# Kernel optimization log

Measured on AMD Instinct MI355X. Metric: run time of the kernel, lower is better.

## Reference

```python
import jax, jax.numpy as jnp
import numpy as np

C, H, D = 64, 2, 32
NQ, NA, NE, F_IN = 8192, 32768, 500000, 128
E_E2Q, E_E2E, E_E2A, E_Q2A = 131072, 800000, 262144, 32768
N_POS, N_NEG = 8192, 24576
# node types: 0=question, 1=answer, 2=entity
# edge types (src_type, dst_type): e2q=(2,0), e2e=(2,2), e2a=(2,1), q2a=(0,1)
REL_ST = [(2, 0), (2, 2), (2, 1), (0, 1)]


def _edges(k, n_src, n_dst, e):
    k1, k2 = jax.random.split(k)
    return jnp.stack([jax.random.randint(k1, (e,), 0, n_src),
                      jax.random.randint(k2, (e,), 0, n_dst)]).astype(jnp.int32)


def setup_inputs():
    key = jax.random.key(0)
    ks = jax.random.split(key, 16)
    inp = {
        'x_question': jax.random.normal(ks[0], (NQ, F_IN), jnp.float32),
        'x_answer': jax.random.normal(ks[1], (NA, F_IN), jnp.float32),
        'x_entity': jax.random.normal(ks[2], (NE, F_IN), jnp.float32),
        'e_e2q': _edges(ks[3], NE, NQ, E_E2Q),
        'e_e2e': _edges(ks[4], NE, NE, E_E2E),
        'e_e2a': _edges(ks[5], NE, NA, E_E2A),
        'e_q2a': _edges(ks[6], NQ, NA, E_Q2A),
        'pos_idx': _edges(ks[7], NQ, NA, N_POS),
        'neg_idx': _edges(ks[8], NQ, NA, N_NEG),
        # learned parameters (stacked over the 3 node types / 4 edge types)
        'W_in': jax.random.normal(ks[9], (3, F_IN, C), jnp.float32) / np.sqrt(F_IN).astype(np.float32),
        'b_in': jnp.zeros((3, C), jnp.float32),
        'bn_gamma': jnp.ones((3, C), jnp.float32),
        'bn_beta': jnp.zeros((3, C), jnp.float32),
        'W_kqv': jax.random.normal(ks[10], (3, C, 3 * C), jnp.float32) / np.sqrt(C).astype(np.float32),
        'b_kqv': jnp.zeros((3, 3 * C), jnp.float32),
        'A_k': jax.random.normal(ks[11], (4, H, D, D), jnp.float32) / np.sqrt(D).astype(np.float32),
        'A_v': jax.random.normal(ks[12], (4, H, D, D), jnp.float32) / np.sqrt(D).astype(np.float32),
        'p_rel': jnp.ones((4, H), jnp.float32),
        'W_out': jax.random.normal(ks[13], (3, C, C), jnp.float32) / np.sqrt(C).astype(np.float32),
        'b_out': jnp.zeros((3, C), jnp.float32),
        'skip': jnp.ones((3,), jnp.float32),
    }
    return inp


def _segment_attn(scores, vals, dst, n):
    # scores [E,H], vals [E,H,D]: softmax over incoming edges per dst node, weighted scatter-add
    m = jax.ops.segment_max(scores, dst, num_segments=n)          # [N,H]
    e = jnp.exp(scores - m[dst])                                   # [E,H]
    s = jax.ops.segment_sum(e, dst, num_segments=n)                # [N,H]
    w = e / s[dst]
    return jax.ops.segment_sum(vals * w[..., None], dst, num_segments=n)  # [N,H,D]


def _forward(x_question, x_answer, x_entity, W_in, b_in, bn_gamma, bn_beta,
             W_kqv, b_kqv, A_k, A_v, p_rel, W_out, b_out, skip, edges):
    xs = [x_question, x_answer, x_entity]
    h = []
    for t in range(3):
        y = jax.nn.relu(xs[t] @ W_in[t] + b_in[t])
        mu = y.mean(0)
        var = y.var(0)  # biased, as in torch BN training mode
        y = bn_gamma[t] * (y - mu) * jax.lax.rsqrt(var + 1e-5) + bn_beta[t]
        h.append(y)
    kqv = [h[t] @ W_kqv[t] + b_kqv[t] for t in range(3)]
    k = [kv[:, :C].reshape(-1, H, D) for kv in kqv]
    q = [kv[:, C:2 * C].reshape(-1, H, D) for kv in kqv]
    v = [kv[:, 2 * C:].reshape(-1, H, D) for kv in kqv]
    by_dst = {0: [], 1: [], 2: []}
    inv_sqrt_d = jnp.float32(1.0 / np.sqrt(D))
    for r, ((st, dt), ei) in enumerate(zip(REL_ST, edges)):
        src, dst = ei[0], ei[1]
        k_r = jnp.einsum('ehd,hdf->ehf', k[st][src], A_k[r])   # per-relation key transform
        v_r = jnp.einsum('ehd,hdf->ehf', v[st][src], A_v[r])   # per-relation value transform
        sc = (q[dt][dst] * k_r).sum(-1) * p_rel[r] * inv_sqrt_d  # [E,H]
        by_dst[dt].append((sc, v_r, dst))
    out = []
    for t in range(3):
        sc = jnp.concatenate([a for a, _, _ in by_dst[t]], axis=0)
        vr = jnp.concatenate([b for _, b, _ in by_dst[t]], axis=0)
        dst = jnp.concatenate([c for _, _, c in by_dst[t]], axis=0)
        n = h[t].shape[0]
        agg = _segment_attn(sc, vr, dst, n).reshape(n, C)
        a = jax.nn.gelu(agg, approximate=False) @ W_out[t] + b_out[t]
        g = jax.nn.sigmoid(skip[t])
        out.append(g * a + (1.0 - g) * h[t])
    return out  # [z_question, z_answer, z_entity]


def reference(x_question, x_answer, x_entity, e_e2q, e_e2e, e_e2a, e_q2a,
              pos_idx, neg_idx, W_in, b_in, bn_gamma, bn_beta, W_kqv, b_kqv,
              A_k, A_v, p_rel, W_out, b_out, skip):
    zq, za, ze = _forward(x_question, x_answer, x_entity, W_in, b_in, bn_gamma,
                          bn_beta, W_kqv, b_kqv, A_k, A_v, p_rel, W_out, b_out,
                          skip, [e_e2q, e_e2e, e_e2a, e_q2a])
    pos_pred = (zq[pos_idx[0]] * za[pos_idx[1]]).sum(-1)
    neg_pred = (zq[neg_idx[0]] * za[neg_idx[1]]).sum(-1)
    return pos_pred, neg_pred, zq, za, ze
```

## Files before the change

### kernel.cpp

```cpp
#include <hip/hip_runtime.h>
#include <hip/hip_bf16.h>
#include <hip/hip_fp16.h>
#include <math.h>

#define NQ 8192
#define NA 32768
#define NE 500000
#define F_IN 128
#define E_E2Q 131072
#define E_E2E 800000
#define E_E2A 262144
#define E_Q2A 32768
#define N_POS 8192
#define N_NEG 24576

#define NT_TOTAL (NQ + NA + NE)
#define E_TOTAL (E_E2Q + E_E2E + E_E2A + E_Q2A)
#define NBLK_SCAN ((NT_TOTAL + 1023) / 1024)
#define CDIV(a, b) (((a) + (b) - 1) / (b))

#define BASE_Q 0
#define BASE_A NQ
#define BASE_E (NQ + NA)

#define GIN_Q 128
#define GIN_A 512
#define GIN_E 768
#define SMEM_INPROJ (32768 + 17408 + 512)

#define GB_Q 2048
#define GB_E 4096
#define GB_A 8192

typedef _Float16 half8_t __attribute__((ext_vector_type(8)));
typedef _Float16 half4_t __attribute__((ext_vector_type(4)));
typedef _Float16 half2_t __attribute__((ext_vector_type(2)));
typedef float f32x4_t __attribute__((ext_vector_type(4)));

__device__ inline void load_lds16(const void* g, void* l) {
  __builtin_amdgcn_global_load_lds((const __attribute__((address_space(1))) void*)g,
                                   (__attribute__((address_space(3))) void*)l, 16, 0, 0);
}

__device__ inline float fast_gelu(float v) {
  float u = 1.5957691216057308f * fmaf(0.044715f * v * v, v, v);
  return v / (1.f + __expf(-u));
}


__global__ __launch_bounds__(256) void prep_misc(
    float* __restrict__ row_start_f,
    const float* __restrict__ W_in, _Float16* __restrict__ WinT,
    const float* __restrict__ W_out, _Float16* __restrict__ WoutT)
{
  int bid = blockIdx.x;
  if (bid < 128) {
    size_t i = (size_t)bid * 256 + threadIdx.x;
    size_t stride = (size_t)128 * 256;
    for (; i < NT_TOTAL; i += stride) row_start_f[i] = 0.f;
  } else if (bid < 320) {
    int b = bid - 128;
    int t = b >> 6, n = b & 63, k = threadIdx.x;
    if (k < 136) {
      float v = (k < 128) ? W_in[(size_t)t * 128 * 64 + (size_t)k * 64 + n] : 0.f;
      WinT[((size_t)t * 64 + n) * 136 + k] = (_Float16)v;
    }
  } else {
    int b = bid - 320;
    int t = b >> 6, n = b & 63, k = threadIdx.x;
    if (k < 72) {
      float v = (k < 64) ? W_out[(size_t)t * 64 * 64 + (size_t)k * 64 + n] : 0.f;
      WoutT[((size_t)t * 64 + n) * 72 + k] = (_Float16)v;
    }
  }
}


__global__ __launch_bounds__(256) void gemm_inproj(
    const float* __restrict__ Af, const _Float16* __restrict__ WT,
    const float* __restrict__ bias, int M, int ntiles,
    _Float16* __restrict__ oh, float* __restrict__ bstats)
{
  extern __shared__ char smem[];
  float* As32 = (float*)smem;
  _Float16* Bs = (_Float16*)(smem + 32768);
  float* s1 = (float*)(smem + 32768 + 17408);
  float* s2 = s1 + 64;

  int tid = threadIdx.x;
  int w = tid >> 6, l = tid & 63;
  int lr = l & 15, lg = l >> 4;

  for (int idx = tid; idx < 64 * 136 / 8; idx += 256)
    *(half8_t*)&Bs[idx * 8] = *(const half8_t*)&WT[(size_t)idx * 8];
  if (tid < 64) { s1[tid] = 0.f; s2[tid] = 0.f; }

  float ps1[4] = {}, ps2[4] = {};
  float bval[4];
#pragma unroll
  for (int ct = 0; ct < 4; ++ct) bval[ct] = bias[ct * 16 + lr];

  for (int tile = blockIdx.x; tile < ntiles; tile += gridDim.x) {
    const char* srcbase = (const char*)Af + (size_t)tile * 64 * 512;
    int rowlim = M - tile * 64;
#pragma unroll
    for (int r = 0; r < 8; ++r) {
      int unit = r * 4 + w;
      char* ldst = (char*)As32 + unit * 1024;
      int p = unit * 1024 + l * 16;
      int row = p >> 9;
      const char* src = (row < rowlim) ? srcbase + (size_t)row * 512 + (p & 511)
                                       : srcbase;
      load_lds16(src, ldst);
    }
    __syncthreads();

    f32x4_t acc[4] = {};
#pragma unroll
    for (int ks = 0; ks < 4; ++ks) {
      const float4* pa = (const float4*)((const char*)As32 +
                          (w * 16 + lr) * 512 + ks * 128 + lg * 32);
      float4 x0 = pa[0], x1 = pa[1];
      half8_t a0 = {(_Float16)x0.x, (_Float16)x0.y, (_Float16)x0.z, (_Float16)x0.w,
                    (_Float16)x1.x, (_Float16)x1.y, (_Float16)x1.z, (_Float16)x1.w};
#pragma unroll
      for (int ct = 0; ct < 4; ++ct) {
        half8_t b = *(const half8_t*)&Bs[(ct * 16 + lr) * 136 + ks * 32 + lg * 8];
        acc[ct] = __builtin_amdgcn_mfma_f32_16x16x32_f16(a0, b, acc[ct], 0, 0, 0);
      }
    }

    int rbase = tile * 64 + w * 16 + lg * 4;
#pragma unroll
    for (int ct = 0; ct < 4; ++ct) {
      int col = ct * 16 + lr;
#pragma unroll
      for (int j = 0; j < 4; ++j) {
        int row = rbase + j;
        if (row >= M) continue;
        float val = fmaxf(acc[ct][j] + bval[ct], 0.f);
        oh[(size_t)row * 64 + col] = (_Float16)val;
        ps1[ct] += val;
        ps2[ct] += val * val;
      }
    }
    __syncthreads();
  }

#pragma unroll
  for (int ct = 0; ct < 4; ++ct) {
    atomicAdd(&s1[ct * 16 + lr], ps1[ct]);
    atomicAdd(&s2[ct * 16 + lr], ps2[ct]);
  }
  __syncthreads();
  if (tid < 64) {
    bstats[(size_t)blockIdx.x * 128 + tid] = s1[tid];
    bstats[(size_t)blockIdx.x * 128 + 64 + tid] = s2[tid];
  }
}


template <int BNT, int KTOT, int MODE>
__global__ __launch_bounds__(256) void gemm_direct(
    const float* __restrict__ Af, const _Float16* __restrict__ Ah,
    const _Float16* __restrict__ WT, const float* __restrict__ bias, int M,
    _Float16* __restrict__ oh, int LDO,
    float* __restrict__ Cf,
    float* __restrict__ bstats,
    const _Float16* __restrict__ resh, const float* __restrict__ rsc,
    const float* __restrict__ rsh, const float* __restrict__ skip_ptr, int skip_idx)
{
  constexpr int KP = KTOT + 8;
  __shared__ _Float16 Bs[BNT * KP];
  int tid = threadIdx.x;
  int w = tid >> 6, l = tid & 63;
  int lr = l & 15, lg = l >> 4;
  int row0 = blockIdx.x * 128;

  for (int idx = tid; idx < BNT * KP / 8; idx += 256)
    *(half8_t*)&Bs[idx * 8] = *(const half8_t*)&WT[(size_t)idx * 8];

  constexpr int NKS = KTOT / 32;
  half8_t afrag[2][NKS];
#pragma unroll
  for (int rt = 0; rt < 2; ++rt) {
    int gr = row0 + w * 32 + rt * 16 + lr;
    bool ok = gr < M;
#pragma unroll
    for (int ks = 0; ks < NKS; ++ks) {
      half8_t h8 = {};
      if (ok) h8 = *(const half8_t*)&Ah[(size_t)gr * KTOT + ks * 32 + lg * 8];
      afrag[rt][ks] = h8;
    }
  }
  __syncthreads();

  constexpr int NCT = BNT / 16;
  f32x4_t acc[2][NCT] = {};
#pragma unroll
  for (int ks = 0; ks < NKS; ++ks) {
#pragma unroll
    for (int ct = 0; ct < NCT; ++ct) {
      half8_t b = *(const half8_t*)&Bs[(ct * 16 + lr) * KP + ks * 32 + lg * 8];
      acc[0][ct] = __builtin_amdgcn_mfma_f32_16x16x32_f16(afrag[0][ks], b, acc[0][ct], 0, 0, 0);
      acc[1][ct] = __builtin_amdgcn_mfma_f32_16x16x32_f16(afrag[1][ks], b, acc[1][ct], 0, 0, 0);
    }
  }

  float g = 1.f / (1.f + __expf(-skip_ptr[skip_idx]));
  float gb = 1.f - g;
#pragma unroll
  for (int rt = 0; rt < 2; ++rt) {
    int rbase = row0 + w * 32 + rt * 16 + lg * 4;
#pragma unroll
    for (int ct = 0; ct < NCT; ++ct) {
      int col = ct * 16 + lr;
      float bval = bias[col];
#pragma unroll
      for (int j = 0; j < 4; ++j) {
        int row = rbase + j;
        if (row >= M) continue;
        float val = acc[rt][ct][j] + bval;
        float rv = (float)resh[(size_t)row * 64 + col];
        Cf[(size_t)row * 64 + col] = g * val + gb * (rsc[col] * rv + rsh[col]);
      }
    }
  }
}


template <int BM, int BNT, int KTOT>
__global__ __launch_bounds__(BM * 2) void gemm_mfma(
    const _Float16* __restrict__ Ah,
    const _Float16* __restrict__ WT, const float* __restrict__ bias, int M,
    _Float16* __restrict__ oh, int LDO)
{
  constexpr int KP = KTOT + 8;
  constexpr int NTHR = BM * 2;
  constexpr int TP = BNT + 8;
  constexpr int SZ_AB = (BM * KP + BNT * KP) * 2;
  constexpr int SZ_T = 128 * TP * 2;
  constexpr int SZ = SZ_AB > SZ_T ? SZ_AB : SZ_T;
  __shared__ __align__(16) char smem[SZ];
  _Float16* As = (_Float16*)smem;
  _Float16* Bs = As + BM * KP;
  _Float16* Ts = (_Float16*)smem;
  int tid = threadIdx.x;
  int row0 = blockIdx.x * BM;
  int colbase = blockIdx.y * BNT;

  {
    constexpr int CH = KTOT / 8;
    for (int idx = tid; idx < BM * CH; idx += NTHR) {
      int row = idx / CH, c = idx % CH;
      int gr = row0 + row;
      half8_t a8 = {};
      if (gr < M) a8 = *(const half8_t*)&Ah[(size_t)gr * KTOT + c * 8];
      *(half8_t*)&As[row * KP + c * 8] = a8;
    }
  }
  {
    const _Float16* wsrc = WT + (size_t)colbase * KP;
    for (int idx = tid; idx < BNT * KP / 8; idx += NTHR)
      *(half8_t*)&Bs[idx * 8] = *(const half8_t*)&wsrc[(size_t)idx * 8];
  }
  __syncthreads();

  int w = tid >> 6, l = tid & 63;
  int lr = l & 15, lg = l >> 4;
  constexpr int NCT = BNT / 16;
  constexpr int NKS = KTOT / 32;
  f32x4_t acc[2][NCT] = {};
#pragma unroll
  for (int ks = 0; ks < NKS; ++ks) {
    half8_t a0 = *(const half8_t*)&As[(w * 32 + lr) * KP + ks * 32 + lg * 8];
    half8_t a1 = *(const half8_t*)&As[(w * 32 + 16 + lr) * KP + ks * 32 + lg * 8];
#pragma unroll
    for (int ct = 0; ct < NCT; ++ct) {
      half8_t b = *(const half8_t*)&Bs[(ct * 16 + lr) * KP + ks * 32 + lg * 8];
      acc[0][ct] = __builtin_amdgcn_mfma_f32_16x16x32_f16(a0, b, acc[0][ct], 0, 0, 0);
      acc[1][ct] = __builtin_amdgcn_mfma_f32_16x16x32_f16(a1, b, acc[1][ct], 0, 0, 0);
    }
  }

  float bval[NCT];
#pragma unroll
  for (int ct = 0; ct < NCT; ++ct) bval[ct] = bias[colbase + ct * 16 + lr];

#pragma unroll
  for (int rt = 0; rt < 2; ++rt) {
    __syncthreads();
    int r2base = w * 16 + lg * 4;
#pragma unroll
    for (int ct = 0; ct < NCT; ++ct) {
      int colL = ct * 16 + lr;
#pragma unroll
      for (int j = 0; j < 4; ++j)
        Ts[(r2base + j) * TP + colL] = (_Float16)(acc[rt][ct][j] + bval[ct]);
    }
    __syncthreads();
    constexpr int C8 = BNT / 8;
    for (int idx = tid; idx < 128 * C8; idx += NTHR) {
      int r2 = idx / C8, c8 = (idx % C8) * 8;
      int gr = row0 + (r2 >> 4) * 32 + rt * 16 + (r2 & 15);
      if (gr < M)
        *(half8_t*)&oh[(size_t)gr * LDO + colbase + c8] = *(const half8_t*)&Ts[r2 * TP + c8];
    }
  }
}


__global__ __launch_bounds__(256) void stats_reduce(const float* __restrict__ bstats,
                                                    float* __restrict__ stats) {
  __shared__ float sh[256];
  int t = blockIdx.x >> 7;
  int c = blockIdx.x & 127;
  int nb = (t == 0) ? GIN_Q : (t == 1) ? GIN_A : GIN_E;
  int base = (t == 0) ? 0 : (t == 1) ? GIN_Q : (GIN_Q + GIN_A);
  float s = 0.f;
  for (int i = threadIdx.x; i < nb; i += 256)
    s += bstats[(size_t)(base + i) * 128 + c];
  sh[threadIdx.x] = s;
  __syncthreads();
  for (int off2 = 128; off2 > 0; off2 >>= 1) {
    if (threadIdx.x < off2) sh[threadIdx.x] += sh[threadIdx.x + off2];
    __syncthreads();
  }
  if (threadIdx.x == 0) stats[t * 128 + c] = sh[0];
}

__global__ void bn_finalize(const float* __restrict__ stats,
                            const float* __restrict__ gamma, const float* __restrict__ beta,
                            float* __restrict__ scale, float* __restrict__ shift) {
  int t = threadIdx.x;
  if (t >= 192) return;
  int ty = t >> 6, c = t & 63;
  float invN = (ty == 0) ? (1.f / NQ) : (ty == 1) ? (1.f / NA) : (1.f / NE);
  float mu = stats[ty * 128 + c] * invN;
  float var = stats[ty * 128 + 64 + c] * invN - mu * mu;
  float rs = rsqrtf(var + 1e-5f);
  float gm = gamma[ty * 64 + c];
  scale[t] = gm * rs;
  shift[t] = beta[ty * 64 + c] - gm * mu * rs;
}

__global__ void kqv_bias2(const float* __restrict__ b_kqv, const float* __restrict__ W_kqv,
                          const float* __restrict__ shift, float* __restrict__ bias2) {
  int t = blockIdx.x, n = threadIdx.x;
  float s = b_kqv[t * 192 + n];
  for (int k = 0; k < 64; ++k)
    s += shift[t * 64 + k] * W_kqv[(size_t)t * 64 * 192 + k * 192 + n];
  bias2[t * 192 + n] = s;
}


__global__ void wprep_kqv(const float* __restrict__ W_kqv, const float* __restrict__ bias2,
                          const float* __restrict__ A_k, const float* __restrict__ A_v,
                          const float* __restrict__ scale,
                          _Float16* __restrict__ WqT, _Float16* __restrict__ WeT,
                          _Float16* __restrict__ WaT, float* __restrict__ bias_big) {
  int j = blockIdx.x;
  int c = threadIdx.x;
  int t, jj, bofs;
  _Float16* W;
  if (j < 192)      { t = 0; jj = j;       W = WqT; bofs = 0; }
  else if (j < 512) { t = 2; jj = j - 192; W = WeT; bofs = 192; }
  else              { t = 1; jj = j - 512; W = WaT; bofs = 512; }
  const float* Wt = W_kqv + (size_t)t * 64 * 192;
  const float* b2 = bias2 + t * 192;
  int mode = 0, rel = 0, sub = 0;
  if (t == 1) { mode = 1; rel = (jj < 64) ? 2 : 3; sub = jj & 63; }
  else if (jj >= 64 && jj < 128) { mode = 1; rel = (t == 0) ? 0 : 1; sub = jj - 64; }
  else if (jj >= 128) {
    mode = 2; sub = (jj - 128) & 63;
    rel = (t == 0) ? 3 : ((jj - 128) >> 6);
  }
  int h = sub >> 5, x = sub & 31;
  float wv, bv;
  if (mode == 0) {
    wv = Wt[(size_t)c * 192 + jj];
    bv = b2[jj];
  } else if (mode == 1) {
    const float* Ar = A_k + ((size_t)rel * 2048 + h * 1024 + x * 32);
    float s = 0.f, sb = 0.f;
    for (int f = 0; f < 32; ++f) {
      float a = Ar[f];
      s = fmaf(a, Wt[(size_t)c * 192 + 64 + h * 32 + f], s);
      sb = fmaf(a, b2[64 + h * 32 + f], sb);
    }
    wv = s; bv = sb;
  } else {
    const float* Ar = A_v + ((size_t)rel * 2048 + h * 1024 + x);
    float s = 0.f, sb = 0.f;
    for (int d = 0; d < 32; ++d) {
      float a = Ar[d * 32];
      s = fmaf(a, Wt[(size_t)c * 192 + 128 + h * 32 + d], s);
      sb = fmaf(a, b2[128 + h * 32 + d], sb);
    }
    wv = s; bv = sb;
  }
  wv *= scale[t * 64 + c];
  W[(size_t)jj * 72 + c] = (_Float16)wv;
  if (c < 8) W[(size_t)jj * 72 + 64 + c] = (_Float16)0.f;
  if (c == 0) bias_big[bofs + jj] = bv;
}


__global__ __launch_bounds__(256) void hist_all(
    const int* __restrict__ d0, const int* __restrict__ d1,
    const int* __restrict__ d2, const int* __restrict__ d3,
    unsigned* __restrict__ cnt)
{
  int i = blockIdx.x * blockDim.x + threadIdx.x;
  int stride = gridDim.x * blockDim.x;
  for (; i < E_TOTAL; i += stride) {
    if (i < E_E2Q) atomicAdd(&cnt[BASE_Q + d0[i]], 1u);
    else if (i < E_E2Q + E_E2E) atomicAdd(&cnt[BASE_E + d1[i - E_E2Q]], 1u);
    else if (i < E_E2Q + E_E2E + E_E2A) atomicAdd(&cnt[BASE_A + d2[i - E_E2Q - E_E2E]], 1u);
    else atomicAdd(&cnt[BASE_A + d3[i - E_E2Q - E_E2E - E_E2A]], 1u);
  }
}

__global__ __launch_bounds__(256) void scan1(unsigned* __restrict__ arr, int n,
                                             unsigned* __restrict__ bsums) {
  __shared__ unsigned sh[256];
  int t = threadIdx.x;
  int base = blockIdx.x * 1024 + t * 4;
  unsigned v[4];
  unsigned s = 0;
#pragma unroll
  for (int j = 0; j < 4; ++j) {
    v[j] = (base + j < n) ? arr[base + j] : 0u;
    s += v[j];
  }
  sh[t] = s;
  __syncthreads();
  for (int off = 1; off < 256; off <<= 1) {
    unsigned x = (t >= off) ? sh[t - off] : 0u;
    __syncthreads();
    sh[t] += x;
    __syncthreads();
  }
  unsigned run = sh[t] - s;
#pragma unroll
  for (int j = 0; j < 4; ++j) {
    if (base + j < n) arr[base + j] = run;
    run += v[j];
  }
  if (t == 255) bsums[blockIdx.x] = sh[255];
}

__global__ __launch_bounds__(256) void scan2(unsigned* __restrict__ bsums, int nb) {
  __shared__ unsigned sh[256];
  __shared__ unsigned carry;
  int t = threadIdx.x;
  if (t == 0) carry = 0;
  __syncthreads();
  for (int chunk = 0; chunk < nb; chunk += 256) {
    int i = chunk + t;
    unsigned v = (i < nb) ? bsums[i] : 0u;
    sh[t] = v;
    __syncthreads();
    for (int off = 1; off < 256; off <<= 1) {
      unsigned x = (t >= off) ? sh[t - off] : 0u;
      __syncthreads();
      sh[t] += x;
      __syncthreads();
    }
    unsigned inc = sh[t];
    unsigned c = carry;
    __syncthreads();
    if (i < nb) bsums[i] = c + inc - v;
    if (t == 255) carry = c + sh[255];
    __syncthreads();
  }
}

__global__ __launch_bounds__(256) void scan3(unsigned* __restrict__ arr,
                                             const unsigned* __restrict__ bsums,
                                             unsigned* __restrict__ cursor, int n) {
  int t = threadIdx.x;
  int base = blockIdx.x * 1024 + t * 4;
  unsigned add = bsums[blockIdx.x];
#pragma unroll
  for (int j = 0; j < 4; ++j) {
    int idx = base + j;
    if (idx < n) {
      unsigned r = arr[idx] + add;
      arr[idx] = r;
      cursor[idx] = r;
    }
  }
}

__global__ __launch_bounds__(256) void scatter_all(
    const int* __restrict__ s0, const int* __restrict__ d0,
    const int* __restrict__ s1, const int* __restrict__ d1,
    const int* __restrict__ s2, const int* __restrict__ d2,
    const int* __restrict__ s3, const int* __restrict__ d3,
    unsigned* __restrict__ cursor, unsigned* __restrict__ eidx)
{
  int i = blockIdx.x * blockDim.x + threadIdx.x;
  int stride = gridDim.x * blockDim.x;
  for (; i < E_TOTAL; i += stride) {
    unsigned pos, pay;
    if (i < E_E2Q) {
      pos = atomicAdd(&cursor[BASE_Q + d0[i]], 1u);
      pay = (unsigned)(s0[i] * 320);
    } else if (i < E_E2Q + E_E2E) {
      int k = i - E_E2Q;
      pos = atomicAdd(&cursor[BASE_E + d1[k]], 1u);
      pay = (unsigned)(s1[k] * 320);
    } else if (i < E_E2Q + E_E2E + E_E2A) {
      int k = i - E_E2Q - E_E2E;
      pos = atomicAdd(&cursor[BASE_A + d2[k]], 1u);
      pay = (unsigned)(s2[k] * 320);
    } else {
      int k = i - E_E2Q - E_E2E - E_E2A;
      pos = atomicAdd(&cursor[BASE_A + d3[k]], 1u);
      pay = (unsigned)(s3[k] * 192) | 0x80000000u;
    }
    eidx[pos] = pay;
  }
}


template <int NREL>
__device__ __forceinline__ void gather_body(
    int bidLocal, int nblocks, int N, int nodebase,
    const unsigned* __restrict__ row_start, const unsigned* __restrict__ row_end,
    const unsigned* __restrict__ eidx,
    const _Float16* __restrict__ baseA, int vofA,
    const _Float16* __restrict__ baseB, int vofB,
    const _Float16* __restrict__ qtA, int ldqA,
    const _Float16* __restrict__ qtB, int ldqB,
    const float* __restrict__ prelA, const float* __restrict__ prelB,
    _Float16* __restrict__ agg)
{
  int lane = threadIdx.x & 63;
  int h = lane >> 5, f = lane & 31;
  int idx2 = h * 32 + 2 * (f & 15);
  const float isd = 0.17677669529663687f;
  float pr0 = prelA[h] * isd;
  float pr1 = (NREL == 2) ? prelB[h] * isd : 0.f;

  int wid = (int)(((size_t)bidLocal * 256 + threadIdx.x) >> 6);
  int nw = nblocks * 4;

  int n0 = wid;
  unsigned b0s = 0, b0e = 0, e00 = 0, e01 = 0;
  half2_t q00p = {}, q01p = {};
  if (n0 < N) {
    b0s = row_start[nodebase + n0];
    b0e = row_end[nodebase + n0];
    q00p = *(const half2_t*)&qtA[(size_t)n0 * ldqA + idx2];
    if (NREL == 2) q01p = *(const half2_t*)&qtB[(size_t)n0 * ldqB + idx2];
    e00 = eidx[b0s];
    e01 = eidx[b0s + 1];
  }
  int n1 = n0 + nw;
  unsigned b1s = 0, b1e = 0;
  half2_t q10p = {}, q11p = {};
  if (n0 < N && n1 < N) {
    b1s = row_start[nodebase + n1];
    b1e = row_end[nodebase + n1];
    q10p = *(const half2_t*)&qtA[(size_t)n1 * ldqA + idx2];
    if (NREL == 2) q11p = *(const half2_t*)&qtB[(size_t)n1 * ldqB + idx2];
  }

  while (n0 < N) {
    unsigned e10 = 0, e11 = 0;
    if (n1 < N) {
      e10 = eidx[b1s];
      e11 = eidx[b1s + 1];
    }
    int n2 = n1 + nw;
    unsigned b2s = 0, b2e = 0;
    half2_t q20p = {}, q21p = {};
    if (n2 < N) {
      b2s = row_start[nodebase + n2];
      b2e = row_end[nodebase + n2];
      q20p = *(const half2_t*)&qtA[(size_t)n2 * ldqA + idx2];
      if (NREL == 2) q21p = *(const half2_t*)&qtB[(size_t)n2 * ldqB + idx2];
    }

    float vs = 0.f, ss = 0.f;
    unsigned i = b0s;

    auto do_pair = [&](unsigned p1, unsigned p2) {
      unsigned o1 = p1 & 0x7FFFFFFFu, o2 = p2 & 0x7FFFFFFFu;
      bool r1 = (NREL == 2) && (p1 >> 31);
      bool r2 = (NREL == 2) && (p2 >> 31);
      const _Float16* b1 = (r1 ? baseB : baseA) + o1;
      const _Float16* b2 = (r2 ? baseB : baseA) + o2;
      half2_t k21 = *(const half2_t*)&b1[idx2];
      float v1 = (float)b1[(r1 ? vofB : vofA) + lane];
      half2_t k22 = *(const half2_t*)&b2[idx2];
      float v2 = (float)b2[(r2 ? vofB : vofA) + lane];
      float sa = __builtin_amdgcn_fdot2(k21, r1 ? q01p : q00p, 0.f, false);
      float sb = __builtin_amdgcn_fdot2(k22, r2 ? q01p : q00p, 0.f, false);
#pragma unroll
      for (int off = 1; off <= 8; off <<= 1) {
        sa += __shfl_xor(sa, off, 32);
        sb += __shfl_xor(sb, off, 32);
      }
      float w1 = __expf(sa * (r1 ? pr1 : pr0));
      float w2 = __expf(sb * (r2 ? pr1 : pr0));
      ss += w1 + w2;
      vs = fmaf(w1, v1, vs);
      vs = fmaf(w2, v2, vs);
    };
    auto do_single = [&](unsigned p1) {
      unsigned o1 = p1 & 0x7FFFFFFFu;
      bool r1 = (NREL == 2) && (p1 >> 31);
      const _Float16* b1 = (r1 ? baseB : baseA) + o1;
      half2_t k21 = *(const half2_t*)&b1[idx2];
      float v1 = (float)b1[(r1 ? vofB : vofA) + lane];
      float sa = __builtin_amdgcn_fdot2(k21, r1 ? q01p : q00p, 0.f, false);
#pragma unroll
      for (int off = 1; off <= 8; off <<= 1) sa += __shfl_xor(sa, off, 32);
      float w1 = __expf(sa * (r1 ? pr1 : pr0));
      ss += w1;
      vs = fmaf(w1, v1, vs);
    };

    if (i + 2 <= b0e) { do_pair(e00, e01); i += 2; }
    else if (i < b0e) { do_single(e00); i = b0e; }
    for (; i + 2 <= b0e; i += 2) do_pair(eidx[i], eidx[i + 1]);
    if (i < b0e) do_single(eidx[i]);

    float val = (ss > 0.f) ? vs / ss : 0.f;
    val = fast_gelu(val);
    agg[((size_t)(nodebase + n0)) * 64 + lane] = (_Float16)val;

    n0 = n1; b0s = b1s; b0e = b1e; q00p = q10p; q01p = q11p; e00 = e10; e01 = e11;
    n1 = n2; b1s = b2s; b1e = b2e; q10p = q20p; q11p = q21p;
  }
}

__global__ __launch_bounds__(256) void gather_all(
    const unsigned* __restrict__ row_start, const unsigned* __restrict__ row_end,
    const unsigned* __restrict__ eidx,
    const _Float16* __restrict__ kqvQ, const _Float16* __restrict__ kqvE,
    const _Float16* __restrict__ kqvA,
    const float* __restrict__ p_rel, _Float16* __restrict__ agg)
{
  int bid = blockIdx.x;
  if (bid < GB_Q) {
    gather_body<1>(bid, GB_Q, NQ, BASE_Q, row_start, row_end, eidx,
                   kqvE, 128, kqvE, 128, kqvQ + 64, 192, kqvQ + 64, 192,
                   p_rel + 0, p_rel + 0, agg);
  } else if (bid < GB_Q + GB_E) {
    gather_body<1>(bid - GB_Q, GB_E, NE, BASE_E, row_start, row_end, eidx,
                   kqvE, 192, kqvE, 192, kqvE + 64, 320, kqvE + 64, 320,
                   p_rel + 2, p_rel + 2, agg);
  } else {
    gather_body<2>(bid - GB_Q - GB_E, GB_A, NA, BASE_A, row_start, row_end, eidx,
                   kqvE, 256, kqvQ, 128, kqvA, 128, kqvA + 64, 128,
                   p_rel + 4, p_rel + 6, agg);
  }
}


__global__ void pred_kernel(const int* __restrict__ qi, const int* __restrict__ ai, int Np,
                            const float* __restrict__ zq, const float* __restrict__ za,
                            float* __restrict__ outp) {
  int i = blockIdx.x * blockDim.x + threadIdx.x;
  if (i >= Np) return;
  const float4* a = (const float4*)(zq + (size_t)qi[i] * 64);
  const float4* b = (const float4*)(za + (size_t)ai[i] * 64);
  float ssum = 0.f;
#pragma unroll
  for (int j = 0; j < 16; ++j) {
    float4 x = a[j], y = b[j];
    ssum += x.x * y.x + x.y * y.y + x.z * y.z + x.w * y.w;
  }
  outp[i] = ssum;
}


extern "C" void kernel_launch(void* const* d_in, const int* in_sizes, int n_in,
                              void* d_out, int out_size, void* d_ws, size_t ws_size,
                              hipStream_t stream) {
  const float* xq = (const float*)d_in[0];
  const float* xa = (const float*)d_in[1];
  const float* xe = (const float*)d_in[2];
  const int* e_e2q = (const int*)d_in[3];
  const int* e_e2e = (const int*)d_in[4];
  const int* e_e2a = (const int*)d_in[5];
  const int* e_q2a = (const int*)d_in[6];
  const int* pos_idx = (const int*)d_in[7];
  const int* neg_idx = (const int*)d_in[8];
  const float* W_in = (const float*)d_in[9];
  const float* b_in = (const float*)d_in[10];
  const float* bn_gamma = (const float*)d_in[11];
  const float* bn_beta = (const float*)d_in[12];
  const float* W_kqv = (const float*)d_in[13];
  const float* b_kqv = (const float*)d_in[14];
  const float* A_k = (const float*)d_in[15];
  const float* A_v = (const float*)d_in[16];
  const float* p_rel = (const float*)d_in[17];
  const float* W_out = (const float*)d_in[18];
  const float* b_out = (const float*)d_in[19];
  const float* skip = (const float*)d_in[20];
  float* out = (float*)d_out;

  float* ws = (float*)d_ws;
  size_t off = 0;
  _Float16* y_h = (_Float16*)(ws + off);    off += (size_t)NT_TOTAL * 32;
  _Float16* kqvQ = (_Float16*)(ws + off);   off += (size_t)NQ * 96;
  _Float16* kqvE = (_Float16*)(ws + off);   off += (size_t)NE * 160;
  _Float16* kqvA = (_Float16*)(ws + off);   off += (size_t)NA * 64;
  _Float16* agg_h = (_Float16*)(ws + off);  off += (size_t)NT_TOTAL * 32;
  float* stats = ws + off;                  off += 384;
  float* scale = ws + off;                  off += 192;
  float* shift = ws + off;                  off += 192;
  float* bias2 = ws + off;                  off += 576;
  float* bias_big = ws + off;               off += 640;
  _Float16* WqT = (_Float16*)(ws + off);    off += 192 * 72 / 2;
  _Float16* WeT = (_Float16*)(ws + off);    off += 320 * 72 / 2;
  _Float16* WaT = (_Float16*)(ws + off);    off += 128 * 72 / 2;
  _Float16* WinT = (_Float16*)(ws + off);   off += 3 * 64 * 136 / 2;
  _Float16* WoutT = (_Float16*)(ws + off);  off += 3 * 64 * 72 / 2;
  float* bstats = ws + off;                 off += (size_t)(GIN_Q + GIN_A + GIN_E) * 128;
  unsigned* row_start = (unsigned*)(ws + off); off += NT_TOTAL;
  unsigned* cursor = (unsigned*)(ws + off);    off += NT_TOTAL;
  unsigned* bsums = (unsigned*)(ws + off);     off += 1024;
  unsigned* eidx = (unsigned*)(ws + off);      off += E_TOTAL + 8;

  const int Ns[3] = {NQ, NA, NE};
  const float* xs[3] = {xq, xa, xe};
  const int gin[3] = {GIN_Q, GIN_A, GIN_E};
  const int bb[3] = {0, GIN_Q, GIN_Q + GIN_A};
  _Float16* yhb[3] = {y_h, y_h + (size_t)NQ * 64, y_h + (size_t)(NQ + NA) * 64};
  _Float16* aggb[3] = {agg_h, agg_h + (size_t)NQ * 64, agg_h + (size_t)(NQ + NA) * 64};
  float* zq_out = out + (N_POS + N_NEG);
  float* zbase[3] = {zq_out, zq_out + (size_t)NQ * 64, zq_out + (size_t)(NQ + NA) * 64};

  prep_misc<<<dim3(512), dim3(256), 0, stream>>>((float*)row_start, W_in, WinT, W_out, WoutT);

  for (int t = 0; t < 3; ++t) {
    gemm_inproj<<<dim3(gin[t]), dim3(256), SMEM_INPROJ, stream>>>(
        xs[t], WinT + (size_t)t * 64 * 136, b_in + t * 64, Ns[t], CDIV(Ns[t], 64),
        yhb[t], bstats + (size_t)bb[t] * 128);
  }
  stats_reduce<<<dim3(384), dim3(256), 0, stream>>>(bstats, stats);
  bn_finalize<<<dim3(1), dim3(192), 0, stream>>>(stats, bn_gamma, bn_beta, scale, shift);
  kqv_bias2<<<dim3(3), dim3(192), 0, stream>>>(b_kqv, W_kqv, shift, bias2);
  wprep_kqv<<<dim3(640), dim3(64), 0, stream>>>(W_kqv, bias2, A_k, A_v, scale,
                                                WqT, WeT, WaT, bias_big);

  gemm_mfma<256, 192, 64><<<dim3(CDIV(NQ, 256)), dim3(512), 0, stream>>>(
      yhb[0], WqT, bias_big, NQ, kqvQ, 192);
  gemm_mfma<256, 160, 64><<<dim3(CDIV(NE, 256), 2), dim3(512), 0, stream>>>(
      yhb[2], WeT, bias_big + 192, NE, kqvE, 320);
  gemm_mfma<256, 128, 64><<<dim3(CDIV(NA, 256)), dim3(512), 0, stream>>>(
      yhb[1], WaT, bias_big + 512, NA, kqvA, 128);

  hist_all<<<dim3(2048), dim3(256), 0, stream>>>(
      e_e2q + E_E2Q, e_e2e + E_E2E, e_e2a + E_E2A, e_q2a + E_Q2A, row_start);
  scan1<<<dim3(NBLK_SCAN), dim3(256), 0, stream>>>(row_start, NT_TOTAL, bsums);
  scan2<<<dim3(1), dim3(256), 0, stream>>>(bsums, NBLK_SCAN);
  scan3<<<dim3(NBLK_SCAN), dim3(256), 0, stream>>>(row_start, bsums, cursor, NT_TOTAL);
  scatter_all<<<dim3(2048), dim3(256), 0, stream>>>(
      e_e2q, e_e2q + E_E2Q, e_e2e, e_e2e + E_E2E,
      e_e2a, e_e2a + E_E2A, e_q2a, e_q2a + E_Q2A, cursor, eidx);

  gather_all<<<dim3(GB_Q + GB_E + GB_A), dim3(256), 0, stream>>>(
      row_start, cursor, eidx, kqvQ, kqvE, kqvA, p_rel, agg_h);

  for (int t = 0; t < 3; ++t) {
    gemm_direct<64, 64, 3><<<dim3(CDIV(Ns[t], 128)), dim3(256), 0, stream>>>(
        nullptr, aggb[t], WoutT + (size_t)t * 64 * 72, b_out + t * 64, Ns[t],
        nullptr, 0, zbase[t], nullptr,
        yhb[t], scale + t * 64, shift + t * 64, skip, t);
  }

  pred_kernel<<<dim3(CDIV(N_POS, 256)), dim3(256), 0, stream>>>(
      pos_idx, pos_idx + N_POS, N_POS, zbase[0], zbase[1], out);
  pred_kernel<<<dim3(CDIV(N_NEG, 256)), dim3(256), 0, stream>>>(
      neg_idx, neg_idx + N_NEG, N_NEG, zbase[0], zbase[1], out + N_POS);
}
```

Before: 728.1 us.

## Merge per-type input/output GEMMs and double-buffer input projection loads

Replaces the three per-node-type input-projection launches with one kernel that dispatches on block index. It double-buffers 32-row input tiles in LDS, issuing async global-to-LDS loads for the next tile while computing the current one. The per-type output GEMM launches and the two prediction launches are likewise each merged into a single launch. The aim is to hide global load latency and cut launch overhead, at the cost of smaller per-iteration tiles and manual waitcnt/barrier synchronisation.

```diff
diff --git a/kernel.cpp b/kernel.cpp
--- a/kernel.cpp
+++ b/kernel.cpp
@@ -26,11 +26,14 @@
 #define GIN_Q 128
 #define GIN_A 512
 #define GIN_E 768
-#define SMEM_INPROJ (32768 + 17408 + 512)
 
 #define GB_Q 2048
 #define GB_E 4096
 #define GB_A 8192
+
+#define TOP_Q 64
+#define TOP_A 256
+#define TOP_E 3907
 
 typedef _Float16 half8_t __attribute__((ext_vector_type(8)));
 typedef _Float16 half4_t __attribute__((ext_vector_type(4)));
@@ -76,64 +79,94 @@
 }
 
 
-__global__ __launch_bounds__(256) void gemm_inproj(
-    const float* __restrict__ Af, const _Float16* __restrict__ WT,
-    const float* __restrict__ bias, int M, int ntiles,
-    _Float16* __restrict__ oh, float* __restrict__ bstats)
+__global__ __launch_bounds__(256) void gemm_inproj_all(
+    const float* __restrict__ xq, const float* __restrict__ xa,
+    const float* __restrict__ xe,
+    const _Float16* __restrict__ WinT, const float* __restrict__ b_in,
+    _Float16* __restrict__ y_h, float* __restrict__ bstats)
 {
-  extern __shared__ char smem[];
-  float* As32 = (float*)smem;
-  _Float16* Bs = (_Float16*)(smem + 32768);
-  float* s1 = (float*)(smem + 32768 + 17408);
-  float* s2 = s1 + 64;
-
-  int tid = threadIdx.x;
-  int w = tid >> 6, l = tid & 63;
+  __shared__ __align__(16) float bufA[32 * 128];
+  __shared__ __align__(16) float bufB[32 * 128];
+  __shared__ _Float16 Bs[64 * 136];
+  __shared__ float s1[64], s2[64];
+
+  int bid = blockIdx.x;
+  int t, lb, nb;
+  const float* Af;
+  _Float16* oh;
+  if (bid < GIN_Q)              { t = 0; lb = bid;                 nb = GIN_Q; Af = xq; oh = y_h; }
+  else if (bid < GIN_Q + GIN_A) { t = 1; lb = bid - GIN_Q;         nb = GIN_A; Af = xa; oh = y_h + (size_t)NQ * 64; }
+  else                          { t = 2; lb = bid - GIN_Q - GIN_A; nb = GIN_E; Af = xe; oh = y_h + (size_t)(NQ + NA) * 64; }
+  int M = (t == 0) ? NQ : (t == 1) ? NA : NE;
+  int nh = CDIV(M, 32);
+  const _Float16* WT = WinT + (size_t)t * 64 * 136;
+  const float* bias = b_in + t * 64;
+
+  int tid = threadIdx.x, w = tid >> 6, l = tid & 63;
   int lr = l & 15, lg = l >> 4;
+  int wrow = (w & 1) * 16;
+  int wcol = (w >> 1) * 32;
 
   for (int idx = tid; idx < 64 * 136 / 8; idx += 256)
     *(half8_t*)&Bs[idx * 8] = *(const half8_t*)&WT[(size_t)idx * 8];
   if (tid < 64) { s1[tid] = 0.f; s2[tid] = 0.f; }
 
-  float ps1[4] = {}, ps2[4] = {};
-  float bval[4];
-#pragma unroll
-  for (int ct = 0; ct < 4; ++ct) bval[ct] = bias[ct * 16 + lr];
-
-  for (int tile = blockIdx.x; tile < ntiles; tile += gridDim.x) {
-    const char* srcbase = (const char*)Af + (size_t)tile * 64 * 512;
-    int rowlim = M - tile * 64;
-#pragma unroll
-    for (int r = 0; r < 8; ++r) {
+  float bval[2];
+  bval[0] = bias[wcol + lr];
+  bval[1] = bias[wcol + 16 + lr];
+  float ps1[2] = {}, ps2[2] = {};
+
+  auto stage = [&](float* buf, int h) {
+    const char* srcbase = (const char*)Af + (size_t)h * 32 * 512;
+    int rowlim = M - h * 32;
+#pragma unroll
+    for (int r = 0; r < 4; ++r) {
       int unit = r * 4 + w;
-      char* ldst = (char*)As32 + unit * 1024;
+      char* ldst = (char*)buf + unit * 1024;
       int p = unit * 1024 + l * 16;
       int row = p >> 9;
       const char* src = (row < rowlim) ? srcbase + (size_t)row * 512 + (p & 511)
                                        : srcbase;
       load_lds16(src, ldst);
     }
-    __syncthreads();
-
-    f32x4_t acc[4] = {};
+  };
+
+  int h0 = lb;
+  if (h0 < nh) stage(bufA, h0);
+  __syncthreads();
+
+  float* cur = bufA;
+  float* nxt = bufB;
+  for (int h = h0; h < nh; h += nb) {
+    int h2 = h + nb;
+    bool more = h2 < nh;
+    if (more) {
+      stage(nxt, h2);
+      asm volatile("s_waitcnt vmcnt(4)" ::: "memory");
+    } else {
+      asm volatile("s_waitcnt vmcnt(0)" ::: "memory");
+    }
+    __builtin_amdgcn_sched_barrier(0);
+    __builtin_amdgcn_s_barrier();
+
+    f32x4_t acc[2] = {};
 #pragma unroll
     for (int ks = 0; ks < 4; ++ks) {
-      const float4* pa = (const float4*)((const char*)As32 +
-                          (w * 16 + lr) * 512 + ks * 128 + lg * 32);
+      const float4* pa = (const float4*)((const char*)cur +
+                          (wrow + lr) * 512 + ks * 128 + lg * 32);
       float4 x0 = pa[0], x1 = pa[1];
       half8_t a0 = {(_Float16)x0.x, (_Float16)x0.y, (_Float16)x0.z, (_Float16)x0.w,
                     (_Float16)x1.x, (_Float16)x1.y, (_Float16)x1.z, (_Float16)x1.w};
 #pragma unroll
-      for (int ct = 0; ct < 4; ++ct) {
-        half8_t b = *(const half8_t*)&Bs[(ct * 16 + lr) * 136 + ks * 32 + lg * 8];
+      for (int ct = 0; ct < 2; ++ct) {
+        half8_t b = *(const half8_t*)&Bs[(wcol + ct * 16 + lr) * 136 + ks * 32 + lg * 8];
         acc[ct] = __builtin_amdgcn_mfma_f32_16x16x32_f16(a0, b, acc[ct], 0, 0, 0);
       }
     }
-
-    int rbase = tile * 64 + w * 16 + lg * 4;
-#pragma unroll
-    for (int ct = 0; ct < 4; ++ct) {
-      int col = ct * 16 + lr;
+    int rbase = h * 32 + wrow + lg * 4;
+#pragma unroll
+    for (int ct = 0; ct < 2; ++ct) {
+      int col = wcol + ct * 16 + lr;
 #pragma unroll
       for (int j = 0; j < 4; ++j) {
         int row = rbase + j;
@@ -144,13 +177,15 @@
         ps2[ct] += val * val;
       }
     }
-    __syncthreads();
-  }
-
-#pragma unroll
-  for (int ct = 0; ct < 4; ++ct) {
-    atomicAdd(&s1[ct * 16 + lr], ps1[ct]);
-    atomicAdd(&s2[ct * 16 + lr], ps2[ct]);
+    __builtin_amdgcn_s_barrier();
+    float* tmp = cur; cur = nxt; nxt = tmp;
+  }
+
+#pragma unroll
+  for (int ct = 0; ct < 2; ++ct) {
+    int col = wcol + ct * 16 + lr;
+    atomicAdd(&s1[col], ps1[ct]);
+    atomicAdd(&s2[col], ps2[ct]);
   }
   __syncthreads();
   if (tid < 64) {
@@ -160,60 +195,66 @@
 }
 
 
-template <int BNT, int KTOT, int MODE>
-__global__ __launch_bounds__(256) void gemm_direct(
-    const float* __restrict__ Af, const _Float16* __restrict__ Ah,
-    const _Float16* __restrict__ WT, const float* __restrict__ bias, int M,
-    _Float16* __restrict__ oh, int LDO,
-    float* __restrict__ Cf,
-    float* __restrict__ bstats,
-    const _Float16* __restrict__ resh, const float* __restrict__ rsc,
-    const float* __restrict__ rsh, const float* __restrict__ skip_ptr, int skip_idx)
+__global__ __launch_bounds__(256) void gemm_out_all(
+    const _Float16* __restrict__ agg_h, const _Float16* __restrict__ y_h,
+    const _Float16* __restrict__ WoutT, const float* __restrict__ b_out,
+    const float* __restrict__ scale, const float* __restrict__ shift,
+    const float* __restrict__ skip, float* __restrict__ zout)
 {
-  constexpr int KP = KTOT + 8;
-  __shared__ _Float16 Bs[BNT * KP];
+  __shared__ _Float16 Bs[64 * 72];
+  int bid = blockIdx.x;
+  int t, row0, M;
+  size_t nodeoff;
+  if (bid < TOP_Q)              { t = 0; row0 = bid * 128;              M = NQ; nodeoff = 0; }
+  else if (bid < TOP_Q + TOP_A) { t = 1; row0 = (bid - TOP_Q) * 128;    M = NA; nodeoff = NQ; }
+  else                          { t = 2; row0 = (bid - TOP_Q - TOP_A) * 128; M = NE; nodeoff = NQ + NA; }
+  const _Float16* Ah = agg_h + nodeoff * 64;
+  const _Float16* resh = y_h + nodeoff * 64;
+  float* Cf = zout + nodeoff * 64;
+  const _Float16* WT = WoutT + (size_t)t * 64 * 72;
+  const float* bias = b_out + t * 64;
+  const float* rsc = scale + t * 64;
+  const float* rsh = shift + t * 64;
+
   int tid = threadIdx.x;
   int w = tid >> 6, l = tid & 63;
   int lr = l & 15, lg = l >> 4;
-  int row0 = blockIdx.x * 128;
-
-  for (int idx = tid; idx < BNT * KP / 8; idx += 256)
+
+  for (int idx = tid; idx < 64 * 72 / 8; idx += 256)
     *(half8_t*)&Bs[idx * 8] = *(const half8_t*)&WT[(size_t)idx * 8];
 
-  constexpr int NKS = KTOT / 32;
-  half8_t afrag[2][NKS];
+  half8_t afrag[2][2];
 #pragma unroll
   for (int rt = 0; rt < 2; ++rt) {
     int gr = row0 + w * 32 + rt * 16 + lr;
     bool ok = gr < M;
 #pragma unroll
-    for (int ks = 0; ks < NKS; ++ks) {
+    for (int ks = 0; ks < 2; ++ks) {
       half8_t h8 = {};
-      if (ok) h8 = *(const half8_t*)&Ah[(size_t)gr * KTOT + ks * 32 + lg * 8];
+      if (ok) h8 = *(const half8_t*)&Ah[(size_t)gr * 64 + ks * 32 + lg * 8];
       afrag[rt][ks] = h8;
     }
   }
   __syncthreads();
 
-  constexpr int NCT = BNT / 16;
-  f32x4_t acc[2][NCT] = {};
-#pragma unroll
-  for (int ks = 0; ks < NKS; ++ks) {
-#pragma unroll
-    for (int ct = 0; ct < NCT; ++ct) {
-      half8_t b = *(const half8_t*)&Bs[(ct * 16 + lr) * KP + ks * 32 + lg * 8];
+  f32x4_t acc[2][4] = {};
+#pragma unroll
+  for (int ks = 0; ks < 2; ++ks) {
+#pragma unroll
+    for (int ct = 0; ct < 4; ++ct) {
+      half8_t b = *(const half8_t*)&Bs[(ct * 16 + lr) * 72 + ks * 32 + lg * 8];
       acc[0][ct] = __builtin_amdgcn_mfma_f32_16x16x32_f16(afrag[0][ks], b, acc[0][ct], 0, 0, 0);
       acc[1][ct] = __builtin_amdgcn_mfma_f32_16x16x32_f16(afrag[1][ks], b, acc[1][ct], 0, 0, 0);
     }
   }
 
-  float g = 1.f / (1.f + __expf(-skip_ptr[skip_idx]));
+  float g = 1.f / (1.f + __expf(-skip[t]));
   float gb = 1.f - g;
 #pragma unroll
   for (int rt = 0; rt < 2; ++rt) {
     int rbase = row0 + w * 32 + rt * 16 + lg * 4;
 #pragma unroll
-    for (int ct = 0; ct < NCT; ++ct) {
+    for (int ct = 0; ct < 4; ++ct) {
       int col = ct * 16 + lr;
       float bval = bias[col];
 #pragma unroll
@@ -662,20 +703,23 @@
 }
 
 
-__global__ void pred_kernel(const int* __restrict__ qi, const int* __restrict__ ai, int Np,
-                            const float* __restrict__ zq, const float* __restrict__ za,
-                            float* __restrict__ outp) {
+__global__ void pred_all(const int* __restrict__ pos, const int* __restrict__ neg,
+                         const float* __restrict__ zq, const float* __restrict__ za,
+                         float* __restrict__ outp) {
   int i = blockIdx.x * blockDim.x + threadIdx.x;
-  if (i >= Np) return;
-  const float4* a = (const float4*)(zq + (size_t)qi[i] * 64);
-  const float4* b = (const float4*)(za + (size_t)ai[i] * 64);
+  if (i >= N_POS + N_NEG) return;
+  int k; const int* qi; const int* ai; float* o;
+  if (i < N_POS) { k = i; qi = pos; ai = pos + N_POS; o = outp; }
+  else { k = i - N_POS; qi = neg; ai = neg + N_NEG; o = outp + N_POS; }
+  const float4* a = (const float4*)(zq + (size_t)qi[k] * 64);
+  const float4* b = (const float4*)(za + (size_t)ai[k] * 64);
   float ssum = 0.f;
 #pragma unroll
   for (int j = 0; j < 16; ++j) {
     float4 x = a[j], y = b[j];
     ssum += x.x * y.x + x.y * y.y + x.z * y.z + x.w * y.w;
   }
-  outp[i] = ssum;
+  o[k] = ssum;
 }
 
 
@@ -728,22 +772,13 @@
   unsigned* bsums = (unsigned*)(ws + off);     off += 1024;
   unsigned* eidx = (unsigned*)(ws + off);      off += E_TOTAL + 8;
 
-  const int Ns[3] = {NQ, NA, NE};
-  const float* xs[3] = {xq, xa, xe};
-  const int gin[3] = {GIN_Q, GIN_A, GIN_E};
-  const int bb[3] = {0, GIN_Q, GIN_Q + GIN_A};
-  _Float16* yhb[3] = {y_h, y_h + (size_t)NQ * 64, y_h + (size_t)(NQ + NA) * 64};
-  _Float16* aggb[3] = {agg_h, agg_h + (size_t)NQ * 64, agg_h + (size_t)(NQ + NA) * 64};
   float* zq_out = out + (N_POS + N_NEG);
-  float* zbase[3] = {zq_out, zq_out + (size_t)NQ * 64, zq_out + (size_t)(NQ + NA) * 64};
 
   prep_misc<<<dim3(512), dim3(256), 0, stream>>>((float*)row_start, W_in, WinT, W_out, WoutT);
 
-  for (int t = 0; t < 3; ++t) {
-    gemm_inproj<<<dim3(gin[t]), dim3(256), SMEM_INPROJ, stream>>>(
-        xs[t], WinT + (size_t)t * 64 * 136, b_in + t * 64, Ns[t], CDIV(Ns[t], 64),
-        yhb[t], bstats + (size_t)bb[t] * 128);
-  }
+  gemm_inproj_all<<<dim3(GIN_Q + GIN_A + GIN_E), dim3(256), 0, stream>>>(
+      xq, xa, xe, WinT, b_in, y_h, bstats);
+
   stats_reduce<<<dim3(384), dim3(256), 0, stream>>>(bstats, stats);
   bn_finalize<<<dim3(1), dim3(192), 0, stream>>>(stats, bn_gamma, bn_beta, scale, shift);
   kqv_bias2<<<dim3(3), dim3(192), 0, stream>>>(b_kqv, W_kqv, shift, bias2);
@@ -751,11 +786,11 @@
                                                 WqT, WeT, WaT, bias_big);
 
   gemm_mfma<256, 192, 64><<<dim3(CDIV(NQ, 256)), dim3(512), 0, stream>>>(
-      yhb[0], WqT, bias_big, NQ, kqvQ, 192);
+      y_h, WqT, bias_big, NQ, kqvQ, 192);
   gemm_mfma<256, 160, 64><<<dim3(CDIV(NE, 256), 2), dim3(512), 0, stream>>>(
-      yhb[2], WeT, bias_big + 192, NE, kqvE, 320);
+      y_h + (size_t)(NQ + NA) * 64, WeT, bias_big + 192, NE, kqvE, 320);
   gemm_mfma<256, 128, 64><<<dim3(CDIV(NA, 256)), dim3(512), 0, stream>>>(
-      yhb[1], WaT, bias_big + 512, NA, kqvA, 128);
+      y_h + (size_t)NQ * 64, WaT, bias_big + 512, NA, kqvA, 128);
 
   hist_all<<<dim3(2048), dim3(256), 0, stream>>>(
       e_e2q + E_E2Q, e_e2e + E_E2E, e_e2a + E_E2A, e_q2a + E_Q2A, row_start);
@@ -769,15 +804,9 @@
   gather_all<<<dim3(GB_Q + GB_E + GB_A), dim3(256), 0, stream>>>(
       row_start, cursor, eidx, kqvQ, kqvE, kqvA, p_rel, agg_h);
 
-  for (int t = 0; t < 3; ++t) {
-    gemm_direct<64, 64, 3><<<dim3(CDIV(Ns[t], 128)), dim3(256), 0, stream>>>(
-        nullptr, aggb[t], WoutT + (size_t)t * 64 * 72, b_out + t * 64, Ns[t],
-        nullptr, 0, zbase[t], nullptr,
-        yhb[t], scale + t * 64, shift + t * 64, skip, t);
-  }
-
-  pred_kernel<<<dim3(CDIV(N_POS, 256)), dim3(256), 0, stream>>>(
-      pos_idx, pos_idx + N_POS, N_POS, zbase[0], zbase[1], out);
-  pred_kernel<<<dim3(CDIV(N_NEG, 256)), dim3(256), 0, stream>>>(
-      neg_idx, neg_idx + N_NEG, N_NEG, zbase[0], zbase[1], out + N_POS);
-}
+  gemm_out_all<<<dim3(TOP_Q + TOP_A + TOP_E), dim3(256), 0, stream>>>(
+      agg_h, y_h, WoutT, b_out, scale, shift, skip, zq_out);
+
+  pred_all<<<dim3(CDIV(N_POS + N_NEG, 256)), dim3(256), 0, stream>>>(
+      pos_idx, neg_idx, zq_out, zq_out + (size_t)NQ * 64, out);
+}
```

After: 709.7 us. 2.5% less time.
